# Kernel optimization log

Hardware: AMD Instinct MI355X
Metric: run time of the kernel (lower is better)

Reference implementation:

```python
import jax, jax.numpy as jnp
import numpy as np

B, WS, DIM, HEADS, AGENT, PS = 128, 14, 256, 8, 49, 7
N = WS * WS


def conv(x, w, b, pad, groups=1):
    y = jax.lax.conv_general_dilated(x, w, (1, 1), [(pad, pad), (pad, pad)],
                                     dimension_numbers=('NCHW', 'OIHW', 'NCHW'),
                                     feature_group_count=groups)
    return y + b[None, :, None, None]


def bilinear_resize(x, oh, ow):
    # F.interpolate(mode='bilinear', align_corners=False) on last two dims
    ih, iw = x.shape[-2], x.shape[-1]
    def grid(ni, no):
        pos = np.maximum((np.arange(no) + 0.5) * (ni / no) - 0.5, 0.0)
        i0 = np.minimum(np.floor(pos).astype(np.int32), ni - 1)
        i1 = np.minimum(i0 + 1, ni - 1)
        return i0, i1, (pos - i0).astype(np.float32)
    i0h, i1h, lh = grid(ih, oh)
    i0w, i1w, lw = grid(iw, ow)
    xh = x[..., i0h, :] * (1.0 - lh)[:, None] + x[..., i1h, :] * lh[:, None]
    return xh[..., i0w] * (1.0 - lw) + xh[..., i1w] * lw


def rel_pos_index(h, w):
    coords = np.stack(np.meshgrid(np.arange(h), np.arange(w), indexing='ij')).reshape(2, -1)
    rel = (coords[:, :, None] - coords[:, None, :]).transpose(1, 2, 0).copy()
    rel[..., 0] += h - 1
    rel[..., 1] += w - 1
    rel[..., 0] *= 2 * w - 1
    return rel.sum(-1)  # (h*w, h*w)


def cbam(x, caa1_w, caa1_b, caa2_w, caa2_b, cam1_w, cam1_b, cam2_w, cam2_b, sa_w, sa_b):
    # ChannelAttention: both conv stacks act on 1x1 pooled maps -> only kernel centers matter
    avgp = x.mean((2, 3))
    t1 = jax.nn.relu(jnp.einsum('oi,bi->bo', caa1_w[:, :, 1, 1], avgp) + caa1_b)
    y1 = jax.nn.sigmoid(jnp.einsum('oi,bi->bo', caa2_w[:, :, 1, 1], t1) + caa2_b)
    mxp = x.max((2, 3))
    t2 = jax.nn.relu(jnp.einsum('oi,bi->bo', cam1_w[:, :, 0, 0], mxp) + cam1_b)
    y2 = jax.nn.sigmoid(jnp.einsum('oi,bi->bo', cam2_w[:, :, 0, 0], t2) + cam2_b)
    x = jax.nn.sigmoid(y1 + y2)[:, :, None, None] * x
    # Spatial attention
    mask = jnp.concatenate([x.mean(1, keepdims=True), x.max(1, keepdims=True)], axis=1)
    mask = jax.nn.sigmoid(conv(mask, sa_w, sa_b, 4))
    return x * mask


def chan_inter(x, ci1_w, ci1_b, bn_g, bn_b, ci2_w, ci2_b):
    # AdaptiveAvgPool2d(1) then 5x5 convs on 1x1 maps -> kernel-center matmuls; BN in eval mode
    p = x.mean((2, 3))
    t = jnp.einsum('oi,bi->bo', ci1_w[:, :, 2, 2], p) + ci1_b
    t = jax.nn.relu(bn_g * t * (1.0 / np.sqrt(1.0 + 1e-5)) + bn_b)
    return jnp.einsum('oi,bi->bo', ci2_w[:, :, 2, 2], t) + ci2_b


def setup_inputs() -> dict:
    key = jax.random.key(0)
    ks = jax.random.split(key, 40)
    d, r = DIM, DIM // 16
    p = lambda i, shape, s=0.02: jax.random.normal(ks[i], shape, jnp.float32) * s
    return {
        'x': jax.random.normal(ks[0], (B, N, d), jnp.float32),
        'h': WS,
        'w': WS,
        'lka_w': p(1, (3 * d, 1, 5, 5)), 'lka_b': p(2, (3 * d,)),
        'conv5_w': p(3, (d, d, 5, 5)), 'conv5_b': p(4, (d,)),
        'caa1_w': p(5, (r, d, 3, 3)), 'caa1_b': p(6, (r,)),
        'caa2_w': p(7, (d, r, 3, 3)), 'caa2_b': p(8, (d,)),
        'cam1_w': p(9, (r, d, 1, 1)), 'cam1_b': p(10, (r,)),
        'cam2_w': p(11, (d, r, 1, 1)), 'cam2_b': p(12, (d,)),
        'sa_w': p(13, (1, 2, 9, 9)), 'sa_b': p(14, (1,)),
        'ci1_w': p(15, (r, d, 5, 5)), 'ci1_b': p(16, (r,)),
        'bn_g': jnp.ones((r,), jnp.float32), 'bn_b': jnp.zeros((r,), jnp.float32),
        'ci2_w': p(17, (d, r, 5, 5)), 'ci2_b': p(18, (d,)),
        'rpb_table': p(19, ((2 * WS - 1) * (2 * WS - 1), HEADS)),
        'an_bias': p(20, (HEADS, AGENT, 7, 7)), 'na_bias': p(21, (HEADS, AGENT, 7, 7)),
        'ah_bias': p(22, (1, HEADS, AGENT, WS, 1)), 'aw_bias': p(23, (1, HEADS, AGENT, 1, WS)),
        'ha_bias': p(24, (1, HEADS, WS, 1, AGENT)), 'wa_bias': p(25, (1, HEADS, 1, WS, AGENT)),
        'dwc_w': p(26, (d, 1, 5, 5)), 'dwc_b': p(27, (d,)),
        'proj_w': p(28, (d, d)), 'proj_b': p(29, (d,)),
    }


def reference(x, h, w, lka_w, lka_b, conv5_w, conv5_b, caa1_w, caa1_b, caa2_w, caa2_b,
              cam1_w, cam1_b, cam2_w, cam2_b, sa_w, sa_b, ci1_w, ci1_b, bn_g, bn_b,
              ci2_w, ci2_b, rpb_table, an_bias, na_bias, ah_bias, aw_bias, ha_bias,
              wa_bias, dwc_w, dwc_b, proj_w, proj_b):
    b, n, c = x.shape
    heads, agent, ps = HEADS, AGENT, PS
    hd = c // heads
    scale = hd ** (-0.5)

    xc = jnp.transpose(x.reshape(b, h, w, c), (0, 3, 1, 2))  # (b,c,h,w)
    y = conv(xc, lka_w, lka_b, 2, groups=c)                   # depthwise, 3 outputs/group
    k_raw, v_raw, q_raw = y[:, :c], y[:, c:2 * c], y[:, 2 * c:]

    # v branch: conv5 then raw reshape-scramble (faithful to torch .reshape of NCHW), then CBAM
    v5 = jnp.transpose(conv(v_raw, conv5_w, conv5_b, 2).reshape(b, h, w, c), (0, 3, 1, 2))
    vc = cbam(v5, caa1_w, caa1_b, caa2_w, caa2_b, cam1_w, cam1_b, cam2_w, cam2_b, sa_w, sa_b)
    v_feat = jnp.transpose(vc.reshape(b, c, n), (0, 2, 1))    # (b,n,c)

    # adaptive avg/max pool 14->7 == exact 2x2 pooling
    at = q_raw.reshape(b, c, ps, h // ps, ps, w // ps).mean((3, 5)).reshape(b, c, agent).transpose(0, 2, 1)
    atk = k_raw.reshape(b, c, ps, h // ps, ps, w // ps).max((3, 5)).reshape(b, c, agent).transpose(0, 2, 1)

    # raw row-major reshapes of (b,c,h,w) into (b,n,heads,hd): faithful to torch
    q = q_raw.reshape(b, n, heads, hd).transpose(0, 2, 1, 3) * scale
    k = k_raw.reshape(b, n, heads, hd).transpose(0, 2, 1, 3)
    v = v_raw.reshape(b, n, heads, hd).transpose(0, 2, 1, 3)
    v1 = v_feat.reshape(b, n, heads, hd).transpose(0, 2, 1, 3)

    # full window attention with relative position bias
    idx = rel_pos_index(h, w)
    rpb = rpb_table[idx.reshape(-1)].reshape(n, n, heads).transpose(2, 0, 1)
    attn = jax.nn.softmax(jnp.einsum('bhid,bhjd->bhij', q, k) + rpb[None])
    x1 = jnp.einsum('bhij,bhjd->bhid', attn, v).transpose(0, 2, 1, 3).reshape(b, n, c)

    ar = x1.transpose(0, 2, 1).reshape(b, c, h, w)
    cmap = chan_inter(ar, ci1_w, ci1_b, bn_g, bn_b, ci2_w, ci2_b)  # (b,c)
    conv_x2 = jax.nn.sigmoid(cmap)[:, :, None, None] * jnp.transpose(q.reshape(b, h, w, c), (0, 3, 1, 2))

    # agent attention
    at_h = at.reshape(b, agent, heads, hd).transpose(0, 2, 1, 3)
    atk_h = atk.reshape(b, agent, heads, hd).transpose(0, 2, 1, 3)
    pb = bilinear_resize(an_bias, h, w).reshape(1, heads, agent, n) \
         + (ah_bias + aw_bias).reshape(1, heads, agent, n)
    agent_attn = jax.nn.softmax(jnp.einsum('bhad,bhnd->bhan', at_h * scale, k) + pb)
    agent_attn1 = jax.nn.softmax(jnp.einsum('bhad,bhnd->bhan', atk_h * scale, q) + pb)
    agent_v = jnp.einsum('bhan,bhnd->bhad', agent_attn, v1) + jnp.einsum('bhan,bhnd->bhad', agent_attn1, v)

    ab = bilinear_resize(na_bias, h, w).reshape(1, heads, agent, n).transpose(0, 1, 3, 2) \
         + (ha_bias + wa_bias).reshape(1, heads, n, agent)
    q_attn = jax.nn.softmax(jnp.einsum('bhnd,bhad->bhna', q * scale, at_h) + ab)
    k_attn = jax.nn.softmax(jnp.einsum('bhnd,bhad->bhna', k * scale, atk_h) + ab)
    xo = jnp.einsum('bhna,bhad->bhnd', q_attn + k_attn, agent_v).transpose(0, 2, 1, 3).reshape(b, n, c)

    xo = xo + jnp.transpose(conv(conv_x2, dwc_w, dwc_b, 2, groups=c), (0, 2, 3, 1)).reshape(b, n, c)
    qc = jnp.transpose(q.transpose(0, 2, 1, 3).reshape(b, h, w, c), (0, 3, 1, 2))
    xo = xo + jnp.transpose(conv(qc, dwc_w, dwc_b, 2, groups=c), (0, 2, 3, 1)).reshape(b, n, c)

    return xo @ proj_w.T + proj_b
```

## Files before the change

kernel.cpp:

```cpp
#include <hip/hip_runtime.h>

#define NB    128
#define NC    256
#define NPOS  196
#define NHEAD 8
#define NAG   49
#define YSTR  150528
#define VOFF  50176
#define QOFF  100352
#define SCL   0.17677669529663687f

#define WS_Y    0u
#define WS_V5   19267584u
#define WS_AT   25690112u
#define WS_ATK  27295744u
#define WS_CHG  28901376u
#define WS_CMAP 28934144u
#define WS_PBT  28966912u
#define WS_AB   29043744u
#define WS_X1S  29120576u
#define WS_AGV  29153344u
#define WS_XO   30758976u
#define WS_WT   37181504u
#define WS_CWT  37247040u

typedef __attribute__((ext_vector_type(8))) _Float16 half8;
typedef __attribute__((ext_vector_type(8))) short short8;
typedef __attribute__((ext_vector_type(4))) short short4v;
typedef __attribute__((ext_vector_type(4))) float f32x4;
typedef unsigned short ushort_t;
typedef unsigned int uint_t;

__device__ __forceinline__ float sigmoidf_(float x){ return 1.0f/(1.0f+__expf(-x)); }

__device__ __forceinline__ ushort_t f2h(float x){
  _Float16 h = (_Float16)x; return __builtin_bit_cast(ushort_t, h);
}
__device__ __forceinline__ float h2f(ushort_t u){
  return (float)__builtin_bit_cast(_Float16, u);
}

__device__ __forceinline__ float bilin7(const float* __restrict__ src, int i, int j){
  float pi = fmaxf(0.5f*(float)i - 0.25f, 0.f);
  int i0 = (int)pi; if (i0 > 6) i0 = 6;
  int i1 = i0 + 1;  if (i1 > 6) i1 = 6;
  float li = pi - (float)i0;
  float pj = fmaxf(0.5f*(float)j - 0.25f, 0.f);
  int j0 = (int)pj; if (j0 > 6) j0 = 6;
  int j1 = j0 + 1;  if (j1 > 6) j1 = 6;
  float lj = pj - (float)j0;
  float v00 = src[i0*7+j0], v01 = src[i0*7+j1];
  float v10 = src[i1*7+j0], v11 = src[i1*7+j1];
  float t0 = v00*(1.f-lj) + v01*lj;
  float t1 = v10*(1.f-lj) + v11*lj;
  return t0*(1.f-li) + t1*li;
}

__device__ __forceinline__ void conv5x5_row(const float* __restrict__ plane, int r,
                                            const float* __restrict__ w25, float* acc14){
  #pragma unroll
  for (int di = 0; di < 5; ++di){
    const float4* pr = (const float4*)(plane + (r+di)*20);
    float4 p0 = pr[0], p1 = pr[1], p2 = pr[2], p3 = pr[3], p4 = pr[4];
    float row[20] = {p0.x,p0.y,p0.z,p0.w, p1.x,p1.y,p1.z,p1.w, p2.x,p2.y,p2.z,p2.w,
                     p3.x,p3.y,p3.z,p3.w, p4.x,p4.y,p4.z,p4.w};
    #pragma unroll
    for (int dj = 0; dj < 5; ++dj){
      float w = w25[di*5+dj];
      #pragma unroll
      for (int j = 0; j < 14; ++j) acc14[j] = fmaf(row[j+dj], w, acc14[j]);
    }
  }
}

__global__ void k_pb(const float* __restrict__ an, const float* __restrict__ ah,
                     const float* __restrict__ aw, float* __restrict__ PBT){
  int t = blockIdx.x*256 + threadIdx.x;
  if (t >= NHEAD*NPOS*NAG) return;
  int a = t % NAG;
  int r = t / NAG;
  int n = r % NPOS;
  int h = r / NPOS;
  int i = n/14, j = n - (n/14)*14;
  float v = bilin7(an + ((size_t)h*NAG + a)*49, i, j);
  v += ah[((size_t)h*NAG + a)*14 + i] + aw[((size_t)h*NAG + a)*14 + j];
  PBT[t] = v;
}

__global__ void k_ab(const float* __restrict__ na, const float* __restrict__ ha,
                     const float* __restrict__ wa, float* __restrict__ AB){
  int t = blockIdx.x*256 + threadIdx.x;
  if (t >= NHEAD*NPOS*NAG) return;
  int a = t % NAG;
  int r = t / NAG;
  int n = r % NPOS;
  int h = r / NPOS;
  int i = n/14, j = n - (n/14)*14;
  float v = bilin7(na + ((size_t)h*NAG + a)*49, i, j);
  v += ha[((size_t)h*14 + i)*NAG + a] + wa[((size_t)h*14 + j)*NAG + a];
  AB[t] = v;
}

__global__ void k_wt(const float* __restrict__ pw, float* __restrict__ WT){
  int t = blockIdx.x*256 + threadIdx.x;
  if (t >= 65536) return;
  int k = t >> 8, c = t & 255;
  WT[t] = pw[c*256 + k];
}

__global__ void k_cw2(const float* __restrict__ cw, ushort_t* __restrict__ Wh){
  int t = blockIdx.x*256 + threadIdx.x;
  if (t >= 1638400) return;
  int ci = t & 255;
  int r  = t >> 8;
  int co = r & 255;
  int tap = r >> 8;
  Wh[t] = f2h(cw[((size_t)co*256 + ci)*25 + tap]);
}

__global__ __launch_bounds__(256) void k_lka(const float* __restrict__ x, const float* __restrict__ lw,
                                             const float* __restrict__ lb, float* __restrict__ Y){
  int b = blockIdx.x >> 3, gb = blockIdx.x & 7;
  int g0 = gb*32;
  __shared__ __align__(16) float pl[32*360];
  int tid = threadIdx.x;
  for (int t = tid; t < 32*360; t += 256) pl[t] = 0.f;
  __syncthreads();
  for (int t = tid; t < 32*196; t += 256){
    int gl = t & 31, s = t >> 5;
    int i = s/14, j = s - i*14;
    pl[gl*360 + (i+2)*20 + j + 2] = x[((size_t)b*196 + s)*256 + g0 + gl];
  }
  __syncthreads();
  for (int t = tid; t < 96*14; t += 256){
    int ocl = t/14, r = t - ocl*14;
    int o  = g0*3 + ocl;
    int gl = ocl/3;
    float w25[25];
    #pragma unroll
    for (int u = 0; u < 25; ++u) w25[u] = lw[o*25 + u];
    float acc[14];
    float bv = lb[o];
    #pragma unroll
    for (int j = 0; j < 14; ++j) acc[j] = bv;
    conv5x5_row(&pl[gl*360], r, w25, acc);
    float* dst = Y + ((size_t)b*768 + o)*196 + r*14;
    #pragma unroll
    for (int j = 0; j < 14; ++j) dst[j] = acc[j];
  }
}

__global__ __launch_bounds__(256, 2) void k_conv5(const float* __restrict__ Y,
    const ushort_t* __restrict__ Wh, const float* __restrict__ cb, float* __restrict__ V5){
  int b = blockIdx.x >> 2, cog = blockIdx.x & 3;
  int co0 = cog*64;
  __shared__ __align__(16) ushort_t Pt[360*40];
  __shared__ __align__(16) ushort_t Wsm[5*64*40];
  __shared__ float T[32*200];
  int tid  = threadIdx.x;
  int lane = tid & 63, wv = tid >> 6;
  int mrow = lane & 15, quad = lane >> 4;

  for (int t = tid; t < 7200; t += 256) ((uint_t*)Pt)[t] = 0;

  int prow[4];
  #pragma unroll
  for (int mt = 0; mt < 4; ++mt){
    int s = wv*64 + mt*16 + mrow;
    int p0 = 0;
    if (s < 196){ int i = s/14, j = s - i*14; p0 = i*20 + j; }
    prow[mt] = p0;
  }

  f32x4 acc[4][4];
  #pragma unroll
  for (int mt = 0; mt < 4; ++mt)
    #pragma unroll
    for (int nt = 0; nt < 4; ++nt) acc[mt][nt] = (f32x4){0.f,0.f,0.f,0.f};

  const float* src = Y + (size_t)b*YSTR + VOFF;
  int wco = tid >> 2, wpart = tid & 3;

  #pragma unroll 1
  for (int cc = 0; cc < 8; ++cc){
    __syncthreads();
    for (int t = tid; t < 784; t += 256){
      int pos = t >> 2, ch = t & 3;
      int i = pos/14, j = pos - i*14;
      int p = (i+2)*20 + j + 2;
      const float* s0 = src + (size_t)(cc*32 + ch*8)*196 + pos;
      short8 pk;
      #pragma unroll
      for (int e = 0; e < 4; ++e){
        float v0 = s0[(2*e)*196];
        float v1 = s0[(2*e+1)*196];
        pk[2*e]   = (short)f2h(v0);
        pk[2*e+1] = (short)f2h(v1);
      }
      *(short8*)&Pt[p*40 + ch*8] = pk;
    }
    #pragma unroll 1
    for (int di = 0; di < 5; ++di){
      __syncthreads();
      #pragma unroll
      for (int tp = 0; tp < 5; ++tp){
        int tap = di*5 + tp;
        const short8 g = *(const short8*)(Wh + ((size_t)tap*256 + co0 + wco)*256 + cc*32 + wpart*8);
        *(short8*)&Wsm[(tp*64 + wco)*40 + wpart*8] = g;
      }
      __syncthreads();
      #pragma unroll
      for (int dj = 0; dj < 5; ++dj){
        half8 a[4], bb[4];
        #pragma unroll
        for (int nt = 0; nt < 4; ++nt){
          int co = nt*16 + mrow;
          bb[nt] = *(const half8*)&Wsm[(dj*64 + co)*40 + quad*8];
        }
        #pragma unroll
        for (int mt = 0; mt < 4; ++mt){
          int p = prow[mt] + di*20 + dj;
          a[mt] = *(const half8*)&Pt[p*40 + quad*8];
        }
        #pragma unroll
        for (int mt = 0; mt < 4; ++mt)
          #pragma unroll
          for (int nt = 0; nt < 4; ++nt)
            acc[mt][nt] = __builtin_amdgcn_mfma_f32_16x16x32_f16(a[mt], bb[nt], acc[mt][nt], 0, 0, 0);
      }
    }
  }

  #pragma unroll
  for (int hf = 0; hf < 2; ++hf){
    __syncthreads();
    #pragma unroll
    for (int ntl = 0; ntl < 2; ++ntl){
      int nt = hf*2 + ntl;
      int col = ntl*16 + mrow;
      #pragma unroll
      for (int mt = 0; mt < 4; ++mt){
        int sbase = wv*64 + mt*16 + quad*4;
        #pragma unroll
        for (int r = 0; r < 4; ++r){
          int s = sbase + r;
          if (s < 196) T[col*200 + s] = acc[mt][nt][r];
        }
      }
    }
    __syncthreads();
    for (int t = tid; t < 6272; t += 256){
      int cl = t / 196;
      int f = (co0 + hf*32)*196 + t;
      float val = T[t + cl*4] + cb[co0 + hf*32 + cl];
      V5[(size_t)b*50176 + (size_t)(f & 255)*196 + (f >> 8)] = val;
    }
  }
}

__global__ __launch_bounds__(256) void k_pool(const float* __restrict__ Y, float* __restrict__ AT, float* __restrict__ ATK){
  int b = blockIdx.x; int c = threadIdx.x;
  const float* qp = Y + ((size_t)b*768 + 512 + c)*196;
  const float* kp = Y + ((size_t)b*768 + c)*196;
  for (int a = 0; a < 49; ++a){
    int p1 = a/7, p2 = a - p1*7;
    int s = p1*28 + p2*2;
    float q0 = qp[s], q1 = qp[s+1], q2 = qp[s+14], q3 = qp[s+15];
    AT[((size_t)b*49 + a)*256 + c] = 0.25f*(q0+q1+q2+q3);
    float k0 = kp[s], k1 = kp[s+1], k2 = kp[s+14], k3 = kp[s+15];
    ATK[((size_t)b*49 + a)*256 + c] = fmaxf(fmaxf(k0,k1), fmaxf(k2,k3));
  }
}

__global__ __launch_bounds__(256) void k_cbam_a(const float* __restrict__ V5,
    const float* __restrict__ caa1w, const float* __restrict__ caa1b,
    const float* __restrict__ caa2w, const float* __restrict__ caa2b,
    const float* __restrict__ cam1w, const float* __restrict__ cam1b,
    const float* __restrict__ cam2w, const float* __restrict__ cam2b,
    float* __restrict__ CHG){
  int b = blockIdx.x, c = threadIdx.x;
  __shared__ float avg[256], mx[256], t1[16], t2[16];
  const float* pp = V5 + ((size_t)b*256 + c)*196;
  float s = 0.f, m = -1e30f;
  for (int i = 0; i < 196; ++i){ float v = pp[i]; s += v; m = fmaxf(m, v); }
  avg[c] = s * (1.0f/196.0f); mx[c] = m;
  __syncthreads();
  if (c < 16){
    float a1 = caa1b[c], a2 = cam1b[c];
    #pragma unroll 4
    for (int k = 0; k < 256; ++k){
      a1 = fmaf(caa1w[(c*256 + k)*9 + 4], avg[k], a1);
      a2 = fmaf(cam1w[c*256 + k], mx[k], a2);
    }
    t1[c] = fmaxf(a1, 0.f);
    t2[c] = fmaxf(a2, 0.f);
  }
  __syncthreads();
  float y1 = caa2b[c], y2 = cam2b[c];
  #pragma unroll
  for (int k = 0; k < 16; ++k){
    y1 = fmaf(caa2w[(c*16 + k)*9 + 4], t1[k], y1);
    y2 = fmaf(cam2w[c*16 + k], t2[k], y2);
  }
  CHG[b*256 + c] = sigmoidf_(sigmoidf_(y1) + sigmoidf_(y2));
}

__global__ __launch_bounds__(256) void k_cbam_b(float* __restrict__ V5, const float* __restrict__ CHG,
    const float* __restrict__ saw, const float* __restrict__ sab){
  int b = blockIdx.x; int tid = threadIdx.x;
  __shared__ float chg[256];
  __shared__ float mp[22*22], xp[22*22];
  __shared__ float mk[196];
  chg[tid] = CHG[b*256 + tid];
  for (int t = tid; t < 484; t += 256){ mp[t] = 0.f; xp[t] = 0.f; }
  __syncthreads();
  if (tid < 196){
    int i = tid/14, j = tid - i*14;
    float s = 0.f, m = -1e30f;
    const float* vb = V5 + (size_t)b*256*196 + tid;
    for (int c = 0; c < 256; ++c){
      float v = chg[c] * vb[c*196];
      s += v; m = fmaxf(m, v);
    }
    mp[(i+4)*22 + j+4] = s*(1.f/256.f);
    xp[(i+4)*22 + j+4] = m;
  }
  __syncthreads();
  if (tid < 196){
    int i = tid/14, j = tid - i*14;
    float acc = sab[0];
    for (int di = 0; di < 9; ++di){
      #pragma unroll
      for (int dj = 0; dj < 9; ++dj){
        acc = fmaf(mp[(i+di)*22 + j+dj], saw[di*9+dj], acc);
        acc = fmaf(xp[(i+di)*22 + j+dj], saw[81 + di*9+dj], acc);
      }
    }
    mk[tid] = sigmoidf_(acc);
  }
  __syncthreads();
  if (tid < 196){
    float m = mk[tid];
    float* vb = V5 + (size_t)b*256*196 + tid;
    for (int c = 0; c < 256; ++c) vb[c*196] = chg[c]*vb[c*196]*m;
  }
}

__global__ __launch_bounds__(512, 1) void k_attn2(const float* __restrict__ Y,
    const float* __restrict__ rpbt, float* __restrict__ X1S){
  int b = blockIdx.x >> 3, h = blockIdx.x & 7;
  __shared__ __align__(16) ushort_t Qh[208*32];
  __shared__ __align__(16) ushort_t Kh[208*32];
  __shared__ __align__(16) ushort_t E[196*208];
  __shared__ float rp[736];
  __shared__ int   rpo[208];
  __shared__ float lnn[208];
  __shared__ float invl[196];
  __shared__ float wj[208];
  __shared__ float wpart[14][208];
  __shared__ float xpart[16][32];
  int tid = threadIdx.x, wv = tid >> 6, lane = tid & 63;
  int mrow = lane & 15, quad = lane >> 4;
  int sw8 = ((quad ^ ((mrow >> 1) & 3)) << 3);
  const float* yb = Y + (size_t)b*YSTR;

  for (int t = tid; t < 736; t += 512) rp[t] = (t < 729) ? rpbt[t*8 + h] : 0.f;
  for (int j = tid; j < 208; j += 512){
    int jc = (j < 196) ? j : 195;
    int rj = jc/14;
    rpo[j] = rj*27 + (jc - rj*14);
  }
  for (int t = tid; t < 384; t += 512){
    int arr = t >= 192; int u = t - arr*192;
    ((uint_t*)(arr ? Kh : Qh))[3136 + u] = 0;
  }
  for (int t = tid; t < 3136; t += 512){
    int n = t >> 4, w = t & 15;
    int ws = (((w >> 2) ^ ((n >> 1) & 3)) << 2) | (w & 3);
    const float2 qv = *(const float2*)(yb + QOFF + (size_t)n*256 + h*32 + (w << 1));
    ((uint_t*)Qh)[n*16 + ws] = (uint_t)f2h(qv.x*SCL) | ((uint_t)f2h(qv.y*SCL) << 16);
    const float2 kv = *(const float2*)(yb + (size_t)n*256 + h*32 + (w << 1));
    ((uint_t*)Kh)[n*16 + ws] = (uint_t)f2h(kv.x) | ((uint_t)f2h(kv.y) << 16);
  }
  __syncthreads();

  #pragma unroll 1
  for (int nc = wv; nc < 13; nc += 8){
    int n = nc*16 + mrow;
    half8 bfr = *(const half8*)&Qh[n*32 + sw8];
    int nclamp = (n < 196) ? n : 195;
    int rin = nclamp/14, cin = nclamp - rin*14;
    int bidxn = (rin + 13)*27 + (cin + 13);
    float lsum = 0.f;
    #pragma unroll 1
    for (int mt = 0; mt < 13; ++mt){
      half8 afr = *(const half8*)&Kh[(mt*16 + mrow)*32 + sw8];
      f32x4 c = (f32x4){0.f,0.f,0.f,0.f};
      c = __builtin_amdgcn_mfma_f32_16x16x32_f16(afr, bfr, c, 0, 0, 0);
      int j0 = mt*16 + quad*4;
      int4 ro = *(const int4*)&rpo[j0];
      short4v pk;
      #pragma unroll
      for (int r = 0; r < 4; ++r){
        int j = j0 + r;
        int roff = (r == 0) ? ro.x : (r == 1) ? ro.y : (r == 2) ? ro.z : ro.w;
        float e = (j < 196) ? __expf(c[r] + rp[bidxn - roff]) : 0.f;
        lsum += e;
        pk[r] = (short)f2h(e);
      }
      if (n < 196) *(short4v*)&E[n*208 + j0] = pk;
    }
    lsum += __shfl_xor(lsum, 16);
    lsum += __shfl_xor(lsum, 32);
    if (quad == 0) lnn[n] = lsum;
  }
  __syncthreads();
  for (int n = tid; n < 196; n += 512) invl[n] = 1.f/lnn[n];
  __syncthreads();

  {
    int g = tid >> 5, lj = tid & 31;
    int j0 = lj*8;
    if (g < 14 && j0 < 208){
      float a0=0.f,a1=0.f,a2=0.f,a3=0.f,a4=0.f,a5=0.f,a6=0.f,a7=0.f;
      #pragma unroll 1
      for (int u = 0; u < 14; ++u){
        int n = g*14 + u;
        float iv = invl[n];
        short8 ev = *(const short8*)&E[n*208 + j0];
        a0 = fmaf(h2f((ushort_t)ev[0]), iv, a0);
        a1 = fmaf(h2f((ushort_t)ev[1]), iv, a1);
        a2 = fmaf(h2f((ushort_t)ev[2]), iv, a2);
        a3 = fmaf(h2f((ushort_t)ev[3]), iv, a3);
        a4 = fmaf(h2f((ushort_t)ev[4]), iv, a4);
        a5 = fmaf(h2f((ushort_t)ev[5]), iv, a5);
        a6 = fmaf(h2f((ushort_t)ev[6]), iv, a6);
        a7 = fmaf(h2f((ushort_t)ev[7]), iv, a7);
      }
      *(f32x4*)&wpart[g][j0]   = (f32x4){a0,a1,a2,a3};
      *(f32x4*)&wpart[g][j0+4] = (f32x4){a4,a5,a6,a7};
    }
  }
  __syncthreads();
  for (int j = tid; j < 208; j += 512){
    float s = 0.f;
    #pragma unroll
    for (int g2 = 0; g2 < 14; ++g2) s += wpart[g2][j];
    wj[j] = (j < 196) ? s : 0.f;
  }
  __syncthreads();

  {
    int d = tid & 31, g = tid >> 5;
    float s = 0.f;
    #pragma unroll 1
    for (int u = 0; u < 13; ++u){
      int j = g*13 + u;
      s = fmaf(wj[j], yb[VOFF + (size_t)j*256 + h*32 + d], s);
    }
    xpart[g][d] = s;
  }
  __syncthreads();
  if (tid < 32){
    float s = 0.f;
    #pragma unroll
    for (int g2 = 0; g2 < 16; ++g2) s += xpart[g2][tid];
    X1S[(size_t)b*256 + h*32 + tid] = s*(1.f/196.f);
  }
}

__global__ __launch_bounds__(256) void k_cinter(const float* __restrict__ X1S,
    const float* __restrict__ ci1w, const float* __restrict__ ci1b,
    const float* __restrict__ bng, const float* __restrict__ bnb,
    const float* __restrict__ ci2w, const float* __restrict__ ci2b, float* __restrict__ CMAP){
  int b = blockIdx.x, c = threadIdx.x;
  __shared__ float p[256], tt[16];
  p[c] = X1S[b*256 + c];
  __syncthreads();
  if (c < 16){
    float a = ci1b[c];
    #pragma unroll 4
    for (int k = 0; k < 256; ++k) a = fmaf(ci1w[(c*256+k)*25 + 12], p[k], a);
    const float invs = 0.9999950000375f;
    tt[c] = fmaxf(fmaf(bng[c]*invs, a, bnb[c]), 0.f);
  }
  __syncthreads();
  float a = ci2b[c];
  #pragma unroll
  for (int k = 0; k < 16; ++k) a = fmaf(ci2w[(c*16+k)*25 + 12], tt[k], a);
  CMAP[b*256 + c] = sigmoidf_(a);
}

__global__ __launch_bounds__(256) void k_agentv(const float* __restrict__ Y, const float* __restrict__ V5,
    const float* __restrict__ AT, const float* __restrict__ ATK,
    const float* __restrict__ PBT, float* __restrict__ AGV){
  int b = blockIdx.x >> 3, h = blockIdx.x & 7;
  __shared__ __align__(16) ushort_t ST[64*232];
  __shared__ __align__(16) ushort_t R[8704];
  __shared__ float psum[4*64];
  __shared__ float inv0s[64], inv1s[64];
  int tid = threadIdx.x, wv = tid >> 6, lane = tid & 63;
  int mrow = lane & 15, quad = lane >> 4;
  int sw8 = ((quad ^ ((mrow >> 1) & 3)) << 3);
  const float* yb = Y + (size_t)b*YSTR;
  ushort_t* Kh = R;
  ushort_t* Ah = R + 6656;
  ushort_t* Vt = R;
  f32x4 out0[2], out1[2];

  for (int t = tid; t < 512; t += 256){
    int a = t >> 3, c2 = 208 + ((t & 7) << 1);
    *(uint_t*)&ST[a*232 + c2] = 0;
  }

  #pragma unroll 1
  for (int pass = 0; pass < 2; ++pass){
    for (int t = tid; t < 192; t += 256) ((uint_t*)Kh)[3136 + t] = 0;
    for (int t = tid; t < 240; t += 256) ((uint_t*)Ah)[784 + t] = 0;
    {
      const float* rsrc = yb + (pass ? QOFF : 0) + h*32;
      for (int t = tid; t < 3136; t += 256){
        int n = t >> 4, w = t & 15;
        const float2 v = *(const float2*)(rsrc + (size_t)n*256 + (w << 1));
        int ws = (((w >> 2) ^ ((n >> 1) & 3)) << 2) | (w & 3);
        ((uint_t*)Kh)[n*16 + ws] = (uint_t)f2h(v.x) | ((uint_t)f2h(v.y) << 16);
      }
      const float* asrc = (pass ? ATK : AT) + (size_t)b*49*256 + h*32;
      for (int t = tid; t < 784; t += 256){
        int a = t >> 4, w = t & 15;
        const float2 v = *(const float2*)(asrc + (size_t)a*256 + (w << 1));
        int ws = (((w >> 2) ^ ((a >> 1) & 3)) << 2) | (w & 3);
        ((uint_t*)Ah)[a*16 + ws] = (uint_t)f2h(v.x) | ((uint_t)f2h(v.y) << 16);
      }
    }
    __syncthreads();
    {
      float lscl = pass ? 0.03125f : SCL;
      int ag = wv*16 + mrow;
      half8 bfr = *(const half8*)&Ah[ag*32 + sw8];
      #pragma unroll 1
      for (int mt = 0; mt < 13; ++mt){
        half8 afr = *(const half8*)&Kh[(mt*16 + mrow)*32 + sw8];
        f32x4 c = (f32x4){0.f,0.f,0.f,0.f};
        c = __builtin_amdgcn_mfma_f32_16x16x32_f16(afr, bfr, c, 0, 0, 0);
        int n0 = mt*16 + quad*4;
        short4v pk;
        #pragma unroll
        for (int r = 0; r < 4; ++r){
          int n = n0 + r;
          float pb = PBT[((size_t)h*196 + n)*49 + ag];
          float e = (n < 196) ? __expf(fmaf(c[r], lscl, pb)) : 0.f;
          pk[r] = (short)f2h(e);
        }
        *(short4v*)&ST[ag*232 + n0] = pk;
      }
    }
    __syncthreads();
    {
      int a = tid >> 2, q = tid & 3;
      float s = 0.f;
      #pragma unroll
      for (int u = 0; u < 7; ++u){
        short8 v8 = *(const short8*)&ST[a*232 + q*56 + u*8];
        #pragma unroll
        for (int e = 0; e < 8; ++e) s += h2f((ushort_t)v8[e]);
      }
      psum[q*64 + a] = s;
    }
    if (pass == 0){
      const float* vsrc = V5 + (size_t)b*50176 + h*32*196;
      for (int t = tid; t < 3136; t += 256){
        int d = t / 98, np = t - (t/98)*98;
        const float2 v = *(const float2*)(vsrc + (size_t)d*196 + 2*np);
        *(uint_t*)&Vt[d*232 + 2*np] = (uint_t)f2h(v.x) | ((uint_t)f2h(v.y) << 16);
      }
    } else {
      const float* vsrc = yb + VOFF + h*32;
      for (int t = tid; t < 3136; t += 256){
        int d = t / 98, np = t - (t/98)*98;
        float v0 = vsrc[(size_t)(2*np)*256 + d];
        float v1 = vsrc[(size_t)(2*np+1)*256 + d];
        *(uint_t*)&Vt[d*232 + 2*np] = (uint_t)f2h(v0) | ((uint_t)f2h(v1) << 16);
      }
    }
    for (int t = tid; t < 448; t += 256){
      int d = t / 14, c2 = 196 + 2*(t - (t/14)*14);
      *(uint_t*)&Vt[d*232 + c2] = 0;
    }
    __syncthreads();
    {
      f32x4* outp = pass ? out1 : out0;
      #pragma unroll
      for (int nt = 0; nt < 2; ++nt){
        f32x4 c = (f32x4){0.f,0.f,0.f,0.f};
        #pragma unroll
        for (int ks = 0; ks < 7; ++ks){
          half8 afr = *(const half8*)&ST[(wv*16 + mrow)*232 + ks*32 + quad*8];
          half8 bfr = *(const half8*)&Vt[(nt*16 + mrow)*232 + ks*32 + quad*8];
          c = __builtin_amdgcn_mfma_f32_16x16x32_f16(afr, bfr, c, 0, 0, 0);
        }
        outp[nt] = c;
      }
      if (tid < 64){
        float s = psum[tid] + psum[64+tid] + psum[128+tid] + psum[192+tid];
        float* invp = pass ? inv1s : inv0s;
        invp[tid] = 1.f / s;
      }
    }
    __syncthreads();
  }
  #pragma unroll
  for (int nt = 0; nt < 2; ++nt){
    int d = nt*16 + mrow;
    #pragma unroll
    for (int r = 0; r < 4; ++r){
      int a = wv*16 + quad*4 + r;
      if (a < 49)
        AGV[(((size_t)(b*8 + h)*49) + a)*32 + d] = out0[nt][r]*inv0s[a] + out1[nt][r]*inv1s[a];
    }
  }
}

__global__ __launch_bounds__(256) void k_xo1(const float* __restrict__ Y,
    const float* __restrict__ AT, const float* __restrict__ ATK,
    const float* __restrict__ AB, const float* __restrict__ AGV, float* __restrict__ XO){
  int b = blockIdx.x >> 3, h = blockIdx.x & 7;
  __shared__ __align__(16) ushort_t ST[208*72];
  __shared__ __align__(16) ushort_t Kh[208*32];
  __shared__ __align__(16) ushort_t Ah[64*32];
  __shared__ __align__(16) ushort_t AGVt[32*64];
  __shared__ float invs[208];
  int tid = threadIdx.x, wv = tid >> 6, lane = tid & 63;
  int mrow = lane & 15, quad = lane >> 4;
  int sw8 = ((quad ^ ((mrow >> 1) & 3)) << 3);
  const float* yb = Y + (size_t)b*YSTR;
  f32x4 acc[4][2];
  #pragma unroll
  for (int i = 0; i < 4; ++i){
    acc[i][0] = (f32x4){0.f,0.f,0.f,0.f};
    acc[i][1] = (f32x4){0.f,0.f,0.f,0.f};
  }

  for (int t = tid; t < 1664; t += 256){
    int rw = t >> 3, c2 = 48 + ((t & 7) << 1);
    *(uint_t*)&ST[rw*72 + c2] = 0;
  }
  {
    const float* agvb = AGV + (size_t)(b*8 + h)*49*32;
    for (int t = tid; t < 2048; t += 256){
      int d = t >> 6, a = t & 63;
      int as = ((((a >> 3) ^ (d & 7)) & 7) << 3) | (a & 7);
      AGVt[d*64 + as] = (a < 49) ? f2h(agvb[a*32 + d]) : (ushort_t)0;
    }
  }

  #pragma unroll 1
  for (int pass = 0; pass < 2; ++pass){
    {
      const float* rsrc = yb + (pass ? 0 : QOFF) + h*32;
      for (int t = tid; t < 3136; t += 256){
        int n = t >> 4, w = t & 15;
        const float2 v = *(const float2*)(rsrc + (size_t)n*256 + (w << 1));
        int ws = (((w >> 2) ^ ((n >> 1) & 3)) << 2) | (w & 3);
        ((uint_t*)Kh)[n*16 + ws] = (uint_t)f2h(v.x) | ((uint_t)f2h(v.y) << 16);
      }
// ... 106 lines not shown
    float w25[25];
    #pragma unroll
    for (int u = 0; u < 25; ++u) w25[u] = dw[c*25 + u];
    float acc[14];
    float b2 = 2.f*db[c];
    #pragma unroll
    for (int j = 0; j < 14; ++j) acc[j] = b2;
    conv5x5_row(&pl[cl*360], r, w25, acc);
    float* dst = XO + ((size_t)b*196 + r*14)*256 + c;
    #pragma unroll
    for (int j = 0; j < 14; ++j) dst[j*256] += acc[j];
  }
}

__global__ __launch_bounds__(256) void k_proj(const float* __restrict__ XO, const float* __restrict__ WT,
    const float* __restrict__ pbias, float* __restrict__ OUT){
  int bb = blockIdx.x / 7, nt = blockIdx.x % 7;
  int n0 = nt*28;
  int c = threadIdx.x;
  const float* xb = XO + ((size_t)bb*196 + n0)*256;
  float acc[28];
  #pragma unroll
  for (int r = 0; r < 28; ++r) acc[r] = 0.f;
  for (int k = 0; k < 256; k += 4){
    float w0 = WT[(k+0)*256 + c];
    float w1 = WT[(k+1)*256 + c];
    float w2 = WT[(k+2)*256 + c];
    float w3 = WT[(k+3)*256 + c];
    #pragma unroll
    for (int r = 0; r < 28; ++r){
      float4 xv = *(const float4*)(xb + r*256 + k);
      acc[r] = fmaf(xv.x, w0, fmaf(xv.y, w1, fmaf(xv.z, w2, fmaf(xv.w, w3, acc[r]))));
    }
  }
  float bv = pbias[c];
  float* dst = OUT + ((size_t)bb*196 + n0)*256 + c;
  #pragma unroll
  for (int r = 0; r < 28; ++r) dst[r*256] = acc[r] + bv;
}

extern "C" void kernel_launch(void* const* d_in, const int* in_sizes, int n_in,
                              void* d_out, int out_size, void* d_ws, size_t ws_size,
                              hipStream_t stream){
  (void)in_sizes; (void)n_in; (void)out_size; (void)ws_size;
  const float* x       = (const float*)d_in[0];
  const float* lka_w   = (const float*)d_in[3];
  const float* lka_b   = (const float*)d_in[4];
  const float* conv5_w = (const float*)d_in[5];
  const float* conv5_b = (const float*)d_in[6];
  const float* caa1_w  = (const float*)d_in[7];
  const float* caa1_b  = (const float*)d_in[8];
  const float* caa2_w  = (const float*)d_in[9];
  const float* caa2_b  = (const float*)d_in[10];
  const float* cam1_w  = (const float*)d_in[11];
  const float* cam1_b  = (const float*)d_in[12];
  const float* cam2_w  = (const float*)d_in[13];
  const float* cam2_b  = (const float*)d_in[14];
  const float* sa_w    = (const float*)d_in[15];
  const float* sa_b    = (const float*)d_in[16];
  const float* ci1_w   = (const float*)d_in[17];
  const float* ci1_b   = (const float*)d_in[18];
  const float* bn_g    = (const float*)d_in[19];
  const float* bn_b    = (const float*)d_in[20];
  const float* ci2_w   = (const float*)d_in[21];
  const float* ci2_b   = (const float*)d_in[22];
  const float* rpbt    = (const float*)d_in[23];
  const float* an_bias = (const float*)d_in[24];
  const float* na_bias = (const float*)d_in[25];
  const float* ah_bias = (const float*)d_in[26];
  const float* aw_bias = (const float*)d_in[27];
  const float* ha_bias = (const float*)d_in[28];
  const float* wa_bias = (const float*)d_in[29];
  const float* dwc_w   = (const float*)d_in[30];
  const float* dwc_b   = (const float*)d_in[31];
  const float* proj_w  = (const float*)d_in[32];
  const float* proj_b  = (const float*)d_in[33];
  float* out = (float*)d_out;
  float* ws = (float*)d_ws;

  float* Y    = ws + WS_Y;
  float* V5   = ws + WS_V5;
  float* AT   = ws + WS_AT;
  float* ATK  = ws + WS_ATK;
  float* CHG  = ws + WS_CHG;
  float* CMAP = ws + WS_CMAP;
  float* PBT  = ws + WS_PBT;
  float* AB   = ws + WS_AB;
  float* X1S  = ws + WS_X1S;
  float* AGV  = ws + WS_AGV;
  float* XO   = ws + WS_XO;
  float* WT   = ws + WS_WT;
  ushort_t* Wh = (ushort_t*)(ws + WS_CWT);

  k_pb   <<<301, 256, 0, stream>>>(an_bias, ah_bias, aw_bias, PBT);
  k_ab   <<<301, 256, 0, stream>>>(na_bias, ha_bias, wa_bias, AB);
  k_wt   <<<256, 256, 0, stream>>>(proj_w, WT);
  k_cw2  <<<6400, 256, 0, stream>>>(conv5_w, Wh);
  k_lka  <<<1024, 256, 0, stream>>>(x, lka_w, lka_b, Y);
  k_conv5<<<512, 256, 0, stream>>>(Y, Wh, conv5_b, V5);
  k_pool <<<128, 256, 0, stream>>>(Y, AT, ATK);
  k_cbam_a<<<128, 256, 0, stream>>>(V5, caa1_w, caa1_b, caa2_w, caa2_b,
                                    cam1_w, cam1_b, cam2_w, cam2_b, CHG);
  k_cbam_b<<<128, 256, 0, stream>>>(V5, CHG, sa_w, sa_b);
  k_attn2<<<1024, 512, 0, stream>>>(Y, rpbt, X1S);
  k_cinter<<<128, 256, 0, stream>>>(X1S, ci1_w, ci1_b, bn_g, bn_b, ci2_w, ci2_b, CMAP);
  k_agentv<<<1024, 256, 0, stream>>>(Y, V5, AT, ATK, PBT, AGV);
  k_xo1  <<<1024, 256, 0, stream>>>(Y, AT, ATK, AB, AGV, XO);
  k_dwc  <<<1024, 256, 0, stream>>>(Y, CMAP, dwc_w, dwc_b, XO);
  k_proj <<<896, 256, 0, stream>>>(XO, WT, proj_b, out);
}
```

Before: 836.1 us.

## Pre-transpose V into fp16 layouts and fuse CBAM kernels with coalesced access

Adds a k_vt kernel that converts the V slice of Y to fp16 once, in two transposed layouts. k_conv5 then loads its input with contiguous 16-byte reads, and k_agentv's second pass copies halves directly instead of doing strided gathers and conversions. The two CBAM kernels are merged into one that reduces per channel with wave shuffles, keeps an fp16 copy of V5 in LDS for the spatial pass, and applies the final scaling with float4 accesses. The trade-offs are an extra launch and an extra memory pass, reuse of the XO workspace as scratch, and fp16 rounding in the CBAM spatial mask statistics.

```diff
diff --git a/kernel.cpp b/kernel.cpp
--- a/kernel.cpp
+++ b/kernel.cpp
@@ -150,7 +150,43 @@
   }
 }
 
-__global__ __launch_bounds__(256, 2) void k_conv5(const float* __restrict__ Y,
+__global__ __launch_bounds__(256) void k_vt(const float* __restrict__ Y,
+    ushort_t* __restrict__ VA, ushort_t* __restrict__ VB){
+  int b = blockIdx.x >> 1, which = blockIdx.x & 1;
+  __shared__ ushort_t L[256*200];
+  int tid = threadIdx.x;
+  const float* src = Y + (size_t)b*YSTR + VOFF;
+  for (int t = tid; t < 25088; t += 256){
+    int f = 2*t;
+    int ci = f/196, pos = f - ci*196;
+    float2 v = *(const float2*)(src + f);
+    *(uint_t*)&L[ci*200 + pos] = (uint_t)f2h(v.x) | ((uint_t)f2h(v.y) << 16);
+  }
+  __syncthreads();
+  if (which == 0){
+    for (int t = tid; t < 6272; t += 256){
+      int pos = t >> 5, ck = (t & 31) << 3;
+      short8 o;
+      #pragma unroll
+      for (int k = 0; k < 8; ++k) o[k] = (short)L[(ck+k)*200 + pos];
+      *(short8*)(VA + (size_t)b*50176 + pos*256 + ck) = o;
+    }
+  } else {
+    for (int t = tid; t < 12544; t += 256){
+      int cp = t / 49, n0 = (t - cp*49)*4;
+      short4v o;
+      #pragma unroll
+      for (int k = 0; k < 4; ++k){
+        int f = (n0+k)*256 + cp;
+        int ci = f/196;
+        o[k] = (short)L[ci*200 + (f - ci*196)];
+      }
+      *(short4v*)(VB + (size_t)b*50176 + cp*196 + n0) = o;
+    }
+  }
+}
+
+__global__ __launch_bounds__(256, 2) void k_conv5(const ushort_t* __restrict__ VA,
     const ushort_t* __restrict__ Wh, const float* __restrict__ cb, float* __restrict__ V5){
   int b = blockIdx.x >> 2, cog = blockIdx.x & 3;
   int co0 = cog*64;
@@ -178,7 +214,7 @@
     #pragma unroll
     for (int nt = 0; nt < 4; ++nt) acc[mt][nt] = (f32x4){0.f,0.f,0.f,0.f};
 
-  const float* src = Y + (size_t)b*YSTR + VOFF;
+  const ushort_t* asrc = VA + (size_t)b*50176;
   int wco = tid >> 2, wpart = tid & 3;
 
   #pragma unroll 1
@@ -188,15 +224,7 @@
       int pos = t >> 2, ch = t & 3;
       int i = pos/14, j = pos - i*14;
       int p = (i+2)*20 + j + 2;
-      const float* s0 = src + (size_t)(cc*32 + ch*8)*196 + pos;
-      short8 pk;
-      #pragma unroll
-      for (int e = 0; e < 4; ++e){
-        float v0 = s0[(2*e)*196];
-        float v1 = s0[(2*e+1)*196];
-        pk[2*e]   = (short)f2h(v0);
-        pk[2*e+1] = (short)f2h(v1);
-      }
+      short8 pk = *(const short8*)(asrc + pos*256 + cc*32 + ch*8);
       *(short8*)&Pt[p*40 + ch*8] = pk;
     }
     #pragma unroll 1
@@ -272,54 +300,70 @@
   }
 }
 
-__global__ __launch_bounds__(256) void k_cbam_a(const float* __restrict__ V5,
+__global__ __launch_bounds__(256) void k_cbam(float* __restrict__ V5,
     const float* __restrict__ caa1w, const float* __restrict__ caa1b,
     const float* __restrict__ caa2w, const float* __restrict__ caa2b,
     const float* __restrict__ cam1w, const float* __restrict__ cam1b,
     const float* __restrict__ cam2w, const float* __restrict__ cam2b,
-    float* __restrict__ CHG){
-  int b = blockIdx.x, c = threadIdx.x;
-  __shared__ float avg[256], mx[256], t1[16], t2[16];
-  const float* pp = V5 + ((size_t)b*256 + c)*196;
-  float s = 0.f, m = -1e30f;
-  for (int i = 0; i < 196; ++i){ float v = pp[i]; s += v; m = fmaxf(m, v); }
-  avg[c] = s * (1.0f/196.0f); mx[c] = m;
-  __syncthreads();
-  if (c < 16){
-    float a1 = caa1b[c], a2 = cam1b[c];
+    const float* __restrict__ saw, const float* __restrict__ sab){
+  int b = blockIdx.x;
+  __shared__ ushort_t vh[256*200];
+  __shared__ float avg[256], mx[256], t1[16], t2[16], chg[256];
+  __shared__ float mp[22*22], xp[22*22];
+  __shared__ __align__(16) float mk[196];
+  int tid = threadIdx.x, wv = tid >> 6, lane = tid & 63;
+  float* v5b = V5 + (size_t)b*50176;
+
+  for (int t = tid; t < 484; t += 256){ mp[t] = 0.f; xp[t] = 0.f; }
+
+  for (int c = wv; c < 256; c += 4){
+    float s, m;
+    if (lane < 49){
+      float4 v = *(const float4*)(v5b + c*196 + lane*4);
+      s = v.x + v.y + v.z + v.w;
+      m = fmaxf(fmaxf(v.x, v.y), fmaxf(v.z, v.w));
+      short4v pk;
+      pk[0] = (short)f2h(v.x); pk[1] = (short)f2h(v.y);
+      pk[2] = (short)f2h(v.z); pk[3] = (short)f2h(v.w);
+      *(short4v*)&vh[c*200 + lane*4] = pk;
+    } else { s = 0.f; m = -1e30f; }
+    #pragma unroll
+    for (int off = 1; off < 64; off <<= 1){
+      s += __shfl_xor(s, off);
+      m = fmaxf(m, __shfl_xor(m, off));
+    }
+    if (lane == 0){ avg[c] = s*(1.0f/196.0f); mx[c] = m; }
+  }
+  __syncthreads();
+
+  if (tid < 16){
+    float a1 = caa1b[tid], a2 = cam1b[tid];
     #pragma unroll 4
     for (int k = 0; k < 256; ++k){
-      a1 = fmaf(caa1w[(c*256 + k)*9 + 4], avg[k], a1);
-      a2 = fmaf(cam1w[c*256 + k], mx[k], a2);
-    }
-    t1[c] = fmaxf(a1, 0.f);
-    t2[c] = fmaxf(a2, 0.f);
-  }
-  __syncthreads();
-  float y1 = caa2b[c], y2 = cam2b[c];
-  #pragma unroll
-  for (int k = 0; k < 16; ++k){
-    y1 = fmaf(caa2w[(c*16 + k)*9 + 4], t1[k], y1);
-    y2 = fmaf(cam2w[c*16 + k], t2[k], y2);
-  }
-  CHG[b*256 + c] = sigmoidf_(sigmoidf_(y1) + sigmoidf_(y2));
-}
-
-__global__ __launch_bounds__(256) void k_cbam_b(float* __restrict__ V5, const float* __restrict__ CHG,
-    const float* __restrict__ saw, const float* __restrict__ sab){
-  int b = blockIdx.x; int tid = threadIdx.x;
-  __shared__ float chg[256];
-  __shared__ float mp[22*22], xp[22*22];
-  __shared__ float mk[196];
-  chg[tid] = CHG[b*256 + tid];
-  for (int t = tid; t < 484; t += 256){ mp[t] = 0.f; xp[t] = 0.f; }
-  __syncthreads();
+      a1 = fmaf(caa1w[(tid*256 + k)*9 + 4], avg[k], a1);
+      a2 = fmaf(cam1w[tid*256 + k], mx[k], a2);
+    }
+    t1[tid] = fmaxf(a1, 0.f);
+    t2[tid] = fmaxf(a2, 0.f);
+  }
+  __syncthreads();
+  {
+    float y1 = caa2b[tid], y2 = cam2b[tid];
+    #pragma unroll
+    for (int k = 0; k < 16; ++k){
+      y1 = fmaf(caa2w[(tid*16 + k)*9 + 4], t1[k], y1);
+      y2 = fmaf(cam2w[tid*16 + k], t2[k], y2);
+    }
+    chg[tid] = sigmoidf_(sigmoidf_(y1) + sigmoidf_(y2));
+  }
+  __syncthreads();
+
   if (tid < 196){
     int i = tid/14, j = tid - i*14;
     float s = 0.f, m = -1e30f;
-    const float* vb = V5 + (size_t)b*256*196 + tid;
+    #pragma unroll 4
     for (int c = 0; c < 256; ++c){
-      float v = chg[c] * vb[c*196];
+      float v = chg[c] * h2f(vh[c*200 + tid]);
       s += v; m = fmaxf(m, v);
     }
     mp[(i+4)*22 + j+4] = s*(1.f/256.f);
@@ -339,10 +383,16 @@
     mk[tid] = sigmoidf_(acc);
   }
   __syncthreads();
-  if (tid < 196){
-    float m = mk[tid];
-    float* vb = V5 + (size_t)b*256*196 + tid;
-    for (int c = 0; c < 256; ++c) vb[c*196] = chg[c]*vb[c*196]*m;
+
+  for (int c = wv; c < 256; c += 4){
+    if (lane < 49){
+      float4 v = *(const float4*)(v5b + c*196 + lane*4);
+      float4 mkv = *(const float4*)&mk[lane*4];
+      float g = chg[c];
+      v.x = g*v.x*mkv.x; v.y = g*v.y*mkv.y;
+      v.z = g*v.z*mkv.z; v.w = g*v.w*mkv.w;
+      *(float4*)(v5b + c*196 + lane*4) = v;
+    }
   }
 }
 
@@ -492,6 +542,7 @@
 }
 
 __global__ __launch_bounds__(256) void k_agentv(const float* __restrict__ Y, const float* __restrict__ V5,
+    const ushort_t* __restrict__ VB,
     const float* __restrict__ AT, const float* __restrict__ ATK,
     const float* __restrict__ PBT, float* __restrict__ AGV){
   int b = blockIdx.x >> 3, h = blockIdx.x & 7;
@@ -575,12 +626,10 @@
         *(uint_t*)&Vt[d*232 + 2*np] = (uint_t)f2h(v.x) | ((uint_t)f2h(v.y) << 16);
       }
     } else {
-      const float* vsrc = yb + VOFF + h*32;
+      const ushort_t* vsrc = VB + (size_t)b*50176 + (h*32)*196;
       for (int t = tid; t < 3136; t += 256){
         int d = t / 98, np = t - (t/98)*98;
-        float v0 = vsrc[(size_t)(2*np)*256 + d];
-        float v1 = vsrc[(size_t)(2*np+1)*256 + d];
-        *(uint_t*)&Vt[d*232 + 2*np] = (uint_t)f2h(v0) | ((uint_t)f2h(v1) << 16);
+        *(uint_t*)&Vt[d*232 + 2*np] = *(const uint_t*)(vsrc + d*196 + 2*np);
       }
     }
     for (int t = tid; t < 448; t += 256){
@@ -853,7 +902,6 @@
   float* V5   = ws + WS_V5;
   float* AT   = ws + WS_AT;
   float* ATK  = ws + WS_ATK;
-  float* CHG  = ws + WS_CHG;
   float* CMAP = ws + WS_CMAP;
   float* PBT  = ws + WS_PBT;
   float* AB   = ws + WS_AB;
@@ -862,20 +910,22 @@
   float* XO   = ws + WS_XO;
   float* WT   = ws + WS_WT;
   ushort_t* Wh = (ushort_t*)(ws + WS_CWT);
+  ushort_t* VA = (ushort_t*)(ws + WS_XO);
+  ushort_t* VB = (ushort_t*)(ws + WS_XO + 3211264u);
 
   k_pb   <<<301, 256, 0, stream>>>(an_bias, ah_bias, aw_bias, PBT);
   k_ab   <<<301, 256, 0, stream>>>(na_bias, ha_bias, wa_bias, AB);
   k_wt   <<<256, 256, 0, stream>>>(proj_w, WT);
   k_cw2  <<<6400, 256, 0, stream>>>(conv5_w, Wh);
   k_lka  <<<1024, 256, 0, stream>>>(x, lka_w, lka_b, Y);
-  k_conv5<<<512, 256, 0, stream>>>(Y, Wh, conv5_b, V5);
+  k_vt   <<<256, 256, 0, stream>>>(Y, VA, VB);
+  k_conv5<<<512, 256, 0, stream>>>(VA, Wh, conv5_b, V5);
   k_pool <<<128, 256, 0, stream>>>(Y, AT, ATK);
-  k_cbam_a<<<128, 256, 0, stream>>>(V5, caa1_w, caa1_b, caa2_w, caa2_b,
-                                    cam1_w, cam1_b, cam2_w, cam2_b, CHG);
-  k_cbam_b<<<128, 256, 0, stream>>>(V5, CHG, sa_w, sa_b);
+  k_cbam <<<128, 256, 0, stream>>>(V5, caa1_w, caa1_b, caa2_w, caa2_b,
+                                   cam1_w, cam1_b, cam2_w, cam2_b, sa_w, sa_b);
   k_attn2<<<1024, 512, 0, stream>>>(Y, rpbt, X1S);
   k_cinter<<<128, 256, 0, stream>>>(X1S, ci1_w, ci1_b, bn_g, bn_b, ci2_w, ci2_b, CMAP);
-  k_agentv<<<1024, 256, 0, stream>>>(Y, V5, AT, ATK, PBT, AGV);
+  k_agentv<<<1024, 256, 0, stream>>>(Y, V5, VB, AT, ATK, PBT, AGV);
   k_xo1  <<<1024, 256, 0, stream>>>(Y, AT, ATK, AB, AGV, XO);
   k_dwc  <<<1024, 256, 0, stream>>>(Y, CMAP, dwc_w, dwc_b, XO);
   k_proj <<<896, 256, 0, stream>>>(XO, WT, proj_b, out);
```

New measurement: 876.9 us. 1.05x slower.

## Tile attention score buffer into row segments and merge bias kernels

Applied to the files above, without the earlier changes.

The window-attention kernel used to keep the full 196x208 half-precision score matrix in shared memory. It now processes query rows in three segments of up to 80 rows, with two waves splitting the key tiles and their partial row sums combined, so shared memory per block drops enough for several blocks per CU (launch bounds 512,4). The two bias-table kernels are merged into one launch, and the pooling kernel is split across twice as many blocks. The price is extra barriers per segment and half-utilized waves in the column reduction.

```diff
diff --git a/kernel.cpp b/kernel.cpp
--- a/kernel.cpp
+++ b/kernel.cpp
@@ -73,32 +73,28 @@
   }
 }
 
-__global__ void k_pb(const float* __restrict__ an, const float* __restrict__ ah,
-                     const float* __restrict__ aw, float* __restrict__ PBT){
-  int t = blockIdx.x*256 + threadIdx.x;
+__global__ void k_pbab(const float* __restrict__ an, const float* __restrict__ ah,
+                       const float* __restrict__ aw, const float* __restrict__ na,
+                       const float* __restrict__ ha, const float* __restrict__ wa,
+                       float* __restrict__ PBT, float* __restrict__ AB){
+  int bid = blockIdx.x;
+  int which = (bid >= 301);
+  int t = (which ? bid - 301 : bid)*256 + threadIdx.x;
   if (t >= NHEAD*NPOS*NAG) return;
   int a = t % NAG;
   int r = t / NAG;
   int n = r % NPOS;
   int h = r / NPOS;
   int i = n/14, j = n - (n/14)*14;
-  float v = bilin7(an + ((size_t)h*NAG + a)*49, i, j);
-  v += ah[((size_t)h*NAG + a)*14 + i] + aw[((size_t)h*NAG + a)*14 + j];
-  PBT[t] = v;
-}
-
-__global__ void k_ab(const float* __restrict__ na, const float* __restrict__ ha,
-                     const float* __restrict__ wa, float* __restrict__ AB){
-  int t = blockIdx.x*256 + threadIdx.x;
-  if (t >= NHEAD*NPOS*NAG) return;
-  int a = t % NAG;
-  int r = t / NAG;
-  int n = r % NPOS;
-  int h = r / NPOS;
-  int i = n/14, j = n - (n/14)*14;
-  float v = bilin7(na + ((size_t)h*NAG + a)*49, i, j);
-  v += ha[((size_t)h*14 + i)*NAG + a] + wa[((size_t)h*14 + j)*NAG + a];
-  AB[t] = v;
+  if (!which){
+    float v = bilin7(an + ((size_t)h*NAG + a)*49, i, j);
+    v += ah[((size_t)h*NAG + a)*14 + i] + aw[((size_t)h*NAG + a)*14 + j];
+    PBT[t] = v;
+  } else {
+    float v = bilin7(na + ((size_t)h*NAG + a)*49, i, j);
+    v += ha[((size_t)h*14 + i)*NAG + a] + wa[((size_t)h*14 + j)*NAG + a];
+    AB[t] = v;
+  }
 }
 
 __global__ void k_wt(const float* __restrict__ pw, float* __restrict__ WT){
@@ -259,10 +255,13 @@
 }
 
 __global__ __launch_bounds__(256) void k_pool(const float* __restrict__ Y, float* __restrict__ AT, float* __restrict__ ATK){
-  int b = blockIdx.x; int c = threadIdx.x;
+  int b = blockIdx.x >> 1, half = blockIdx.x & 1;
+  int c = (threadIdx.x & 127) + half*128;
+  int a0 = (threadIdx.x >> 7) ? 25 : 0;
+  int a1 = (threadIdx.x >> 7) ? 49 : 25;
   const float* qp = Y + ((size_t)b*768 + 512 + c)*196;
   const float* kp = Y + ((size_t)b*768 + c)*196;
-  for (int a = 0; a < 49; ++a){
+  for (int a = a0; a < a1; ++a){
     int p1 = a/7, p2 = a - p1*7;
     int s = p1*28 + p2*2;
     float q0 = qp[s], q1 = qp[s+1], q2 = qp[s+14], q3 = qp[s+15];
@@ -346,18 +345,18 @@
   }
 }
 
-__global__ __launch_bounds__(512, 1) void k_attn2(const float* __restrict__ Y,
+__global__ __launch_bounds__(512, 4) void k_attn3(const float* __restrict__ Y,
     const float* __restrict__ rpbt, float* __restrict__ X1S){
   int b = blockIdx.x >> 3, h = blockIdx.x & 7;
   __shared__ __align__(16) ushort_t Qh[208*32];
   __shared__ __align__(16) ushort_t Kh[208*32];
-  __shared__ __align__(16) ushort_t E[196*208];
+  __shared__ __align__(16) ushort_t E[80*208];
   __shared__ float rp[736];
   __shared__ int   rpo[208];
-  __shared__ float lnn[208];
-  __shared__ float invl[196];
+  __shared__ float pl2[80][2];
+  __shared__ float invl[80];
   __shared__ float wj[208];
-  __shared__ float wpart[14][208];
+  __shared__ float wpart[8][208];
   __shared__ float xpart[16][32];
   int tid = threadIdx.x, wv = tid >> 6, lane = tid & 63;
   int mrow = lane & 15, quad = lane >> 4;
@@ -369,6 +368,7 @@
     int jc = (j < 196) ? j : 195;
     int rj = jc/14;
     rpo[j] = rj*27 + (jc - rj*14);
+    wj[j] = 0.f;
   }
   for (int t = tid; t < 384; t += 512){
     int arr = t >= 192; int u = t - arr*192;
@@ -384,71 +384,75 @@
   }
   __syncthreads();
 
+  int mt0 = (wv & 1) ? 7 : 0;
+  int mt1 = (wv & 1) ? 13 : 7;
+
   #pragma unroll 1
-  for (int nc = wv; nc < 13; nc += 8){
-    int n = nc*16 + mrow;
-    half8 bfr = *(const half8*)&Qh[n*32 + sw8];
-    int nclamp = (n < 196) ? n : 195;
-    int rin = nclamp/14, cin = nclamp - rin*14;
-    int bidxn = (rin + 13)*27 + (cin + 13);
-    float lsum = 0.f;
+  for (int seg = 0; seg < 3; ++seg){
+    int base = (seg == 0) ? 0 : (seg == 1) ? 80 : 144;
+    int ntl  = (seg == 0) ? 5 : 4;
+    int segrows = ntl*16;
+    int vrows = 196 - base; if (vrows > segrows) vrows = segrows;
+
     #pragma unroll 1
-    for (int mt = 0; mt < 13; ++mt){
-      half8 afr = *(const half8*)&Kh[(mt*16 + mrow)*32 + sw8];
-      f32x4 c = (f32x4){0.f,0.f,0.f,0.f};
-      c = __builtin_amdgcn_mfma_f32_16x16x32_f16(afr, bfr, c, 0, 0, 0);
-      int j0 = mt*16 + quad*4;
-      int4 ro = *(const int4*)&rpo[j0];
-      short4v pk;
-      #pragma unroll
-      for (int r = 0; r < 4; ++r){
-        int j = j0 + r;
-        int roff = (r == 0) ? ro.x : (r == 1) ? ro.y : (r == 2) ? ro.z : ro.w;
-        float e = (j < 196) ? __expf(c[r] + rp[bidxn - roff]) : 0.f;
-        lsum += e;
-        pk[r] = (short)f2h(e);
-      }
-      if (n < 196) *(short4v*)&E[n*208 + j0] = pk;
-    }
-    lsum += __shfl_xor(lsum, 16);
-    lsum += __shfl_xor(lsum, 32);
-    if (quad == 0) lnn[n] = lsum;
-  }
-  __syncthreads();
-  for (int n = tid; n < 196; n += 512) invl[n] = 1.f/lnn[n];
-  __syncthreads();
-
-  {
-    int g = tid >> 5, lj = tid & 31;
-    int j0 = lj*8;
-    if (g < 14 && j0 < 208){
-      float a0=0.f,a1=0.f,a2=0.f,a3=0.f,a4=0.f,a5=0.f,a6=0.f,a7=0.f;
+    for (int ncl = (wv >> 1); ncl < ntl; ncl += 4){
+      int n = base + ncl*16 + mrow;
+      half8 bfr = *(const half8*)&Qh[n*32 + sw8];
+      int nclamp = (n < 196) ? n : 195;
+      int rin = nclamp/14, cin = nclamp - rin*14;
+      int bidxn = (rin + 13)*27 + (cin + 13);
+      float lsum = 0.f;
       #pragma unroll 1
-      for (int u = 0; u < 14; ++u){
-        int n = g*14 + u;
-        float iv = invl[n];
-        short8 ev = *(const short8*)&E[n*208 + j0];
-        a0 = fmaf(h2f((ushort_t)ev[0]), iv, a0);
-        a1 = fmaf(h2f((ushort_t)ev[1]), iv, a1);
-        a2 = fmaf(h2f((ushort_t)ev[2]), iv, a2);
-        a3 = fmaf(h2f((ushort_t)ev[3]), iv, a3);
-        a4 = fmaf(h2f((ushort_t)ev[4]), iv, a4);
-        a5 = fmaf(h2f((ushort_t)ev[5]), iv, a5);
-        a6 = fmaf(h2f((ushort_t)ev[6]), iv, a6);
-        a7 = fmaf(h2f((ushort_t)ev[7]), iv, a7);
-      }
-      *(f32x4*)&wpart[g][j0]   = (f32x4){a0,a1,a2,a3};
-      *(f32x4*)&wpart[g][j0+4] = (f32x4){a4,a5,a6,a7};
-    }
-  }
-  __syncthreads();
-  for (int j = tid; j < 208; j += 512){
-    float s = 0.f;
-    #pragma unroll
-    for (int g2 = 0; g2 < 14; ++g2) s += wpart[g2][j];
-    wj[j] = (j < 196) ? s : 0.f;
-  }
-  __syncthreads();
+      for (int mt = mt0; mt < mt1; ++mt){
+        half8 afr = *(const half8*)&Kh[(mt*16 + mrow)*32 + sw8];
+        f32x4 c = (f32x4){0.f,0.f,0.f,0.f};
+        c = __builtin_amdgcn_mfma_f32_16x16x32_f16(afr, bfr, c, 0, 0, 0);
+        int j0 = mt*16 + quad*4;
+        int4 ro = *(const int4*)&rpo[j0];
+        short4v pk;
+        #pragma unroll
+        for (int r = 0; r < 4; ++r){
+          int j = j0 + r;
+          int roff = (r == 0) ? ro.x : (r == 1) ? ro.y : (r == 2) ? ro.z : ro.w;
+          float e = (j < 196) ? __expf(c[r] + rp[bidxn - roff]) : 0.f;
+          lsum += e;
+          pk[r] = (short)f2h(e);
+        }
+        if (n < 196) *(short4v*)&E[(n - base)*208 + j0] = pk;
+      }
+      lsum += __shfl_xor(lsum, 16);
+      lsum += __shfl_xor(lsum, 32);
+      if (quad == 0) pl2[n - base][wv & 1] = lsum;
+    }
+    __syncthreads();
+    for (int t = tid; t < vrows; t += 512) invl[t] = 1.f/(pl2[t][0] + pl2[t][1]);
+    __syncthreads();
+
+    {
+      int j0 = lane*4;
+      if (j0 < 208){
+        float a0=0.f,a1=0.f,a2=0.f,a3=0.f;
+        #pragma unroll 1
+        for (int nl = wv; nl < vrows; nl += 8){
+          float iv = invl[nl];
+          short4v ev = *(const short4v*)&E[nl*208 + j0];
+          a0 = fmaf(h2f((ushort_t)ev[0]), iv, a0);
+          a1 = fmaf(h2f((ushort_t)ev[1]), iv, a1);
+          a2 = fmaf(h2f((ushort_t)ev[2]), iv, a2);
+          a3 = fmaf(h2f((ushort_t)ev[3]), iv, a3);
+        }
+        *(f32x4*)&wpart[wv][j0] = (f32x4){a0,a1,a2,a3};
+      }
+    }
+    __syncthreads();
+    for (int j = tid; j < 208; j += 512){
+      float s = wj[j];
+      #pragma unroll
+      for (int g = 0; g < 8; ++g) s += wpart[g][j];
+      wj[j] = s;
+    }
+    __syncthreads();
+  }
 
   {
     int d = tid & 31, g = tid >> 5;
@@ -863,17 +867,16 @@
   float* WT   = ws + WS_WT;
   ushort_t* Wh = (ushort_t*)(ws + WS_CWT);
 
-  k_pb   <<<301, 256, 0, stream>>>(an_bias, ah_bias, aw_bias, PBT);
-  k_ab   <<<301, 256, 0, stream>>>(na_bias, ha_bias, wa_bias, AB);
+  k_pbab <<<602, 256, 0, stream>>>(an_bias, ah_bias, aw_bias, na_bias, ha_bias, wa_bias, PBT, AB);
   k_wt   <<<256, 256, 0, stream>>>(proj_w, WT);
   k_cw2  <<<6400, 256, 0, stream>>>(conv5_w, Wh);
   k_lka  <<<1024, 256, 0, stream>>>(x, lka_w, lka_b, Y);
   k_conv5<<<512, 256, 0, stream>>>(Y, Wh, conv5_b, V5);
-  k_pool <<<128, 256, 0, stream>>>(Y, AT, ATK);
+  k_pool <<<256, 256, 0, stream>>>(Y, AT, ATK);
   k_cbam_a<<<128, 256, 0, stream>>>(V5, caa1_w, caa1_b, caa2_w, caa2_b,
                                     cam1_w, cam1_b, cam2_w, cam2_b, CHG);
   k_cbam_b<<<128, 256, 0, stream>>>(V5, CHG, sa_w, sa_b);
-  k_attn2<<<1024, 512, 0, stream>>>(Y, rpbt, X1S);
+  k_attn3<<<1024, 512, 0, stream>>>(Y, rpbt, X1S);
   k_cinter<<<128, 256, 0, stream>>>(X1S, ci1_w, ci1_b, bn_g, bn_b, ci2_w, ci2_b, CMAP);
   k_agentv<<<1024, 256, 0, stream>>>(Y, V5, AT, ATK, PBT, AGV);
   k_xo1  <<<1024, 256, 0, stream>>>(Y, AT, ATK, AB, AGV, XO);
```

Measured after the change: 812.4 us. 1.03x faster.
